# Performance work log

Hardware: AMD Instinct MI355X
Metric: run time of the kernel (lower is better)

The kernel has to match this reference:

```python
import jax, jax.numpy as jnp
import numpy as np
from jax import lax

D_MODEL = 128; HEADS = 4; HEAD_DIM = 32
D_INNER = 256; STATE = 16; KCONV = 4; DT_RANK = 8
N_T = 2; N_M = 6
B = 4; L = 2048; D_IN = 256
EPS = 1e-5


def build_layer_schedule(nt, nm):
    total = nt + nm
    sched = []
    t = 0
    for i in range(total):
        tgt = (i + 1) * nt / total
        if t < tgt and t < nt:
            sched.append('transformer'); t += 1
        else:
            sched.append('mamba')
    return sched


def ln(x, s, b):
    mu = x.mean(-1, keepdims=True)
    v = ((x - mu) ** 2).mean(-1, keepdims=True)
    return (x - mu) * lax.rsqrt(v + EPS) * s + b


def transformer_layer(h, in_w, in_b, out_w, out_b, w1, b1, w2, b2, n1s, n1b, n2s, n2b):
    # torch TransformerEncoderLayer, batch_first, post-norm, relu, dropout=eval(off)
    Bb, S, D = h.shape
    qkv = h @ in_w.T + in_b
    q, k, v = jnp.split(qkv, 3, axis=-1)
    def heads(t):
        return t.reshape(Bb, S, HEADS, HEAD_DIM).transpose(0, 2, 1, 3)
    q, k, v = heads(q), heads(k), heads(v)
    scores = jnp.einsum('bhqd,bhkd->bhqk', q, k) / np.float32(np.sqrt(HEAD_DIM))
    attn = jax.nn.softmax(scores, axis=-1)
    o = jnp.einsum('bhqk,bhkd->bhqd', attn, v).transpose(0, 2, 1, 3).reshape(Bb, S, D)
    o = o @ out_w.T + out_b
    h = ln(h + o, n1s, n1b)
    ff = jax.nn.relu(h @ w1.T + b1) @ w2.T + b2
    return ln(h + ff, n2s, n2b)


def mamba_block(h, ns, nb, in_w, conv_w, conv_b, xp_w, dt_w, dt_b, A_log, Dp, out_w):
    xn = ln(h, ns, nb)
    xz = xn @ in_w.T  # [B,L,2*Di]
    x, z = jnp.split(xz, 2, axis=-1)
    Lseq = x.shape[1]
    # causal depthwise conv1d (pad left K-1, truncate to L)
    xpad = jnp.pad(x, ((0, 0), (KCONV - 1, 0), (0, 0)))
    x = sum(xpad[:, k:k + Lseq, :] * conv_w[:, k] for k in range(KCONV)) + conv_b
    x = jax.nn.silu(x)
    # input-dependent dt, B, C
    dbc = x @ xp_w.T  # [B,L,R+2N]
    dt_r = dbc[..., :DT_RANK]
    Bm = dbc[..., DT_RANK:DT_RANK + STATE]
    Cm = dbc[..., DT_RANK + STATE:]
    dt = jax.nn.softplus(dt_r @ dt_w.T + dt_b)  # [B,L,Di]
    A = -jnp.exp(A_log)  # [Di,N]
    dA = jnp.exp(dt[..., None] * A)               # [B,L,Di,N]
    dBu = (dt * x)[..., None] * Bm[:, :, None, :]  # [B,L,Di,N]

    def step(hstate, inp):
        dA_t, dBu_t, C_t = inp
        hstate = dA_t * hstate + dBu_t
        return hstate, jnp.einsum('bdn,bn->bd', hstate, C_t)

    h0 = jnp.zeros((x.shape[0], D_INNER, STATE), x.dtype)
    _, ys = lax.scan(step, h0, (dA.swapaxes(0, 1), dBu.swapaxes(0, 1), Cm.swapaxes(0, 1)))
    y = ys.swapaxes(0, 1) + x * Dp
    y = y * jax.nn.silu(z)
    return h + y @ out_w.T


def setup_inputs() -> dict:
    key = jax.random.key(0)
    ks = jax.random.split(key, 12)
    def rn(k, shape, s=0.02):
        return jax.random.normal(k, shape, dtype=jnp.float32) * s
    return {
        'x': jax.random.normal(ks[0], (B, L, D_IN), dtype=jnp.float32),
        'proj_w': rn(ks[1], (D_MODEL, D_IN)),
        'proj_b': jnp.zeros((D_MODEL,), jnp.float32),
        't_in_w': rn(ks[2], (N_T, 3 * D_MODEL, D_MODEL)),
        't_in_b': jnp.zeros((N_T, 3 * D_MODEL), jnp.float32),
        't_out_w': rn(ks[3], (N_T, D_MODEL, D_MODEL)),
        't_out_b': jnp.zeros((N_T, D_MODEL), jnp.float32),
        't_ff1_w': rn(ks[4], (N_T, 4 * D_MODEL, D_MODEL)),
        't_ff1_b': jnp.zeros((N_T, 4 * D_MODEL), jnp.float32),
        't_ff2_w': rn(ks[5], (N_T, D_MODEL, 4 * D_MODEL)),
        't_ff2_b': jnp.zeros((N_T, D_MODEL), jnp.float32),
        't_n1_s': jnp.ones((N_T, D_MODEL), jnp.float32),
        't_n1_b': jnp.zeros((N_T, D_MODEL), jnp.float32),
        't_n2_s': jnp.ones((N_T, D_MODEL), jnp.float32),
        't_n2_b': jnp.zeros((N_T, D_MODEL), jnp.float32),
        'm_norm_s': jnp.ones((N_M, D_MODEL), jnp.float32),
        'm_norm_b': jnp.zeros((N_M, D_MODEL), jnp.float32),
        'm_in_w': rn(ks[6], (N_M, 2 * D_INNER, D_MODEL)),
        'm_conv_w': rn(ks[7], (N_M, D_INNER, KCONV), 0.2),
        'm_conv_b': jnp.zeros((N_M, D_INNER), jnp.float32),
        'm_xproj_w': rn(ks[8], (N_M, DT_RANK + 2 * STATE, D_INNER)),
        'm_dt_w': rn(ks[9], (N_M, D_INNER, DT_RANK)),
        'm_dt_b': jnp.full((N_M, D_INNER), -2.0, jnp.float32),
        'm_A_log': jnp.log(jnp.broadcast_to(jnp.arange(1, STATE + 1, dtype=jnp.float32), (N_M, D_INNER, STATE))),
        'm_D': jnp.ones((N_M, D_INNER), jnp.float32),
        'm_out_w': rn(ks[10], (N_M, D_MODEL, D_INNER)),
        'norm_s': jnp.ones((D_MODEL,), jnp.float32),
        'norm_b': jnp.zeros((D_MODEL,), jnp.float32),
    }


def reference(x, proj_w, proj_b, t_in_w, t_in_b, t_out_w, t_out_b, t_ff1_w, t_ff1_b, t_ff2_w, t_ff2_b, t_n1_s, t_n1_b, t_n2_s, t_n2_b, m_norm_s, m_norm_b, m_in_w, m_conv_w, m_conv_b, m_xproj_w, m_dt_w, m_dt_b, m_A_log, m_D, m_out_w, norm_s, norm_b):
    h = x @ proj_w.T + proj_b
    ti = mi = 0
    for kind in build_layer_schedule(N_T, N_M):
        if kind == 'transformer':
            h = transformer_layer(h, t_in_w[ti], t_in_b[ti], t_out_w[ti], t_out_b[ti], t_ff1_w[ti], t_ff1_b[ti], t_ff2_w[ti], t_ff2_b[ti], t_n1_s[ti], t_n1_b[ti], t_n2_s[ti], t_n2_b[ti])
            ti += 1
        else:
            h = mamba_block(h, m_norm_s[mi], m_norm_b[mi], m_in_w[mi], m_conv_w[mi], m_conv_b[mi], m_xproj_w[mi], m_dt_w[mi], m_dt_b[mi], m_A_log[mi], m_D[mi], m_out_w[mi])
            mi += 1
    return ln(h, norm_s, norm_b)
```

## Files before the change

kernel.cpp:

```cpp
#include <hip/hip_runtime.h>
#include <hip/hip_bf16.h>
#include <math.h>

using bf16 = __hip_bfloat16;

typedef __attribute__((ext_vector_type(8))) short short8;
typedef __attribute__((ext_vector_type(4))) short short4v;
typedef __attribute__((ext_vector_type(4))) float float4v;

#define BATCH 4
#define SEQL 2048
#define TOK (BATCH * SEQL)
#define NCHUNK 128
#define TCHUNK 16
#define PSOFF ((size_t)BATCH * NCHUNK * 256 * 16)
#define NSPLIT 2

#define NPAR 28
#define PAR_TOTAL 3227264

struct Srcs { const void* p[NPAR]; int off[NPAR + 1]; };

__device__ __forceinline__ short f2b(float f) {
    unsigned u = __builtin_bit_cast(unsigned, f);
    unsigned r = (u + 0x7FFF + ((u >> 16) & 1)) >> 16;
    return (short)r;
}
__device__ __forceinline__ float b2f(short s) {
    unsigned u = ((unsigned)(unsigned short)s) << 16;
    return __builtin_bit_cast(float, u);
}
__device__ __forceinline__ unsigned pk2t(float a, float b) {
    unsigned ua = __builtin_bit_cast(unsigned, a);
    unsigned ub = __builtin_bit_cast(unsigned, b);
    return (ub & 0xFFFF0000u) | (ua >> 16);
}

__global__ __launch_bounds__(128) void sniff_kernel(const unsigned int* __restrict__ xw,
                                                    int* __restrict__ flag) {
    __shared__ int cnt;
    if (threadIdx.x == 0) cnt = 0;
    __syncthreads();
    unsigned u = xw[threadIdx.x];
    unsigned elo = (u >> 7) & 0xFF;
    unsigned ehi = (u >> 23) & 0xFF;
    int ok = (elo >= 100 && elo <= 140) && (ehi >= 100 && ehi <= 140);
    if (ok) atomicAdd(&cnt, 1);
    __syncthreads();
    if (threadIdx.x == 0) *flag = (cnt >= 96) ? 1 : 0;
}

__global__ __launch_bounds__(256) void cvt_all(Srcs s, const int* __restrict__ flag,
                                               short* __restrict__ dstb, int total) {
    int idx = blockIdx.x * 256 + threadIdx.x;
    if (idx >= total) return;
    int t = 0;
    while (idx >= s.off[t + 1]) ++t;
    int j = idx - s.off[t];
    dstb[idx] = (*flag) ? ((const short*)s.p[t])[j]
                        : f2b(((const float*)s.p[t])[j]);
}

__global__ __launch_bounds__(256) void gemm_gen(const short* __restrict__ A,
                                                const short* __restrict__ W,
                                                const short* __restrict__ bias,
                                                short* __restrict__ Cb,
                                                int N, int K, int lda, int act) {
    __shared__ short As[64][72];
    __shared__ short Bs[64][72];
    const int bm = blockIdx.y * 64, bn = blockIdx.x * 64;
    const int tid = threadIdx.x;
    const int w = tid >> 6, lane = tid & 63;
    const int la = lane & 15, quad = lane >> 4;
    const int srow = tid >> 2, sk0 = (tid & 3) * 16;
    short8 av0, av1, bv0, bv1;
    {
        const short* ap = A + (size_t)(bm + srow) * lda + sk0;
        const short* wp = W + (size_t)(bn + srow) * K + sk0;
        av0 = *(const short8*)ap;
        av1 = *(const short8*)(ap + 8);
        bv0 = *(const short8*)wp;
        bv1 = *(const short8*)(wp + 8);
    }
    float4v acc[4] = {};
    #pragma unroll 1
    for (int kb = 0; kb < K; kb += 64) {
        *(short4v*)&As[srow][sk0]      = *(short4v*)&av0;
        *(short4v*)&As[srow][sk0 + 4]  = *((short4v*)&av0 + 1);
        *(short4v*)&As[srow][sk0 + 8]  = *(short4v*)&av1;
        *(short4v*)&As[srow][sk0 + 12] = *((short4v*)&av1 + 1);
        *(short4v*)&Bs[srow][sk0]      = *(short4v*)&bv0;
        *(short4v*)&Bs[srow][sk0 + 4]  = *((short4v*)&bv0 + 1);
        *(short4v*)&Bs[srow][sk0 + 8]  = *(short4v*)&bv1;
        *(short4v*)&Bs[srow][sk0 + 12] = *((short4v*)&bv1 + 1);
        __syncthreads();
        if (kb + 64 < K) {
            const short* ap = A + (size_t)(bm + srow) * lda + kb + 64 + sk0;
            const short* wp = W + (size_t)(bn + srow) * K + kb + 64 + sk0;
            av0 = *(const short8*)ap;
            av1 = *(const short8*)(ap + 8);
            bv0 = *(const short8*)wp;
            bv1 = *(const short8*)(wp + 8);
        }
        #pragma unroll
        for (int ks = 0; ks < 2; ++ks) {
            short8 af;
            *(short4v*)&af       = *(short4v*)&As[w * 16 + la][ks * 32 + quad * 8];
            *((short4v*)&af + 1) = *(short4v*)&As[w * 16 + la][ks * 32 + quad * 8 + 4];
            #pragma unroll
            for (int f = 0; f < 4; ++f) {
                short8 bf;
                *(short4v*)&bf       = *(short4v*)&Bs[f * 16 + la][ks * 32 + quad * 8];
                *((short4v*)&bf + 1) = *(short4v*)&Bs[f * 16 + la][ks * 32 + quad * 8 + 4];
                acc[f] = __builtin_amdgcn_mfma_f32_16x16x32_bf16(af, bf, acc[f], 0, 0, 0);
            }
        }
        __syncthreads();
    }
    #pragma unroll
    for (int f = 0; f < 4; ++f) {
        int n = bn + f * 16 + la;
        float bv = bias ? b2f(bias[n]) : 0.f;
        #pragma unroll
        for (int i = 0; i < 4; ++i) {
            int m = bm + w * 16 + quad * 4 + i;
            float v = acc[f][i] + bv;
            if (act == 1) v = fmaxf(v, 0.f);
            Cb[(size_t)m * N + n] = f2b(v);
        }
    }
}

__global__ __launch_bounds__(256) void gemm128(const short* __restrict__ A,
                                               const short* __restrict__ W,
                                               const short* __restrict__ bias,
                                               const float* __restrict__ res,
                                               const short* __restrict__ s1,
                                               const short* __restrict__ b1,
                                               const short* __restrict__ s2,
                                               const short* __restrict__ b2,
                                               float* __restrict__ outH,
                                               short* __restrict__ outHb,
                                               short* __restrict__ outX,
                                               int K, int lda,
                                               const short* __restrict__ OpSrc,
                                               const float* __restrict__ ML) {
    __shared__ short As[32][72];
    __shared__ short Bs[128][72];
    __shared__ short Ac[32][136];
    __shared__ float pS[2][34];
    __shared__ float pQ[2][34];
    const int bm = blockIdx.x * 32;
    const int tid = threadIdx.x;
    const int w = tid >> 6, lane = tid & 63;
    const int la = lane & 15, quad = lane >> 4;
    const int wr = w & 1, wc = w >> 1;
    if (OpSrc) {
        const int row = tid >> 3, c0 = (tid & 7) * 16;
        const int tok = bm + row;
        float den = 0.f;
        #pragma unroll
        for (int s = 0; s < NSPLIT; ++s) den += ML[(size_t)s * TOK + tok];
        const float inv = 1.f / den;
        #pragma unroll
        for (int cc = 0; cc < 16; cc += 8) {
            float num[8] = {};
            #pragma unroll
            for (int s = 0; s < NSPLIT; ++s) {
                short8 v = *(const short8*)(OpSrc + ((size_t)s * TOK + tok) * 128 + c0 + cc);
                #pragma unroll
                for (int j = 0; j < 8; ++j) num[j] += b2f(v[j]);
            }
            #pragma unroll
            for (int j = 0; j < 8; ++j) Ac[row][c0 + cc + j] = f2b(num[j] * inv);
        }
        __syncthreads();
    }
    const int br = tid >> 1, bh2 = (tid & 1) * 32;
    short8 breg[4];
    {
        const short* wp = W + (size_t)br * K + bh2;
        #pragma unroll
        for (int j = 0; j < 4; ++j) breg[j] = *(const short8*)(wp + j * 8);
    }
    float4v acc[4] = {};
    #pragma unroll 1
    for (int kb = 0; kb < K; kb += 64) {
        if (!OpSrc) {
            const int row = tid >> 3, k0 = (tid & 7) * 8;
            const short* ap = A + (size_t)(bm + row) * lda + kb + k0;
            short8 a0 = *(const short8*)ap;
            *(short4v*)&As[row][k0]     = *(short4v*)&a0;
            *(short4v*)&As[row][k0 + 4] = *((short4v*)&a0 + 1);
        }
        #pragma unroll
        for (int j = 0; j < 4; ++j) {
            *(short4v*)&Bs[br][bh2 + j * 8]     = *(short4v*)&breg[j];
            *(short4v*)&Bs[br][bh2 + j * 8 + 4] = *((short4v*)&breg[j] + 1);
        }
        __syncthreads();
        if (kb + 64 < K) {
            const short* wp = W + (size_t)br * K + kb + 64 + bh2;
            #pragma unroll
            for (int j = 0; j < 4; ++j) breg[j] = *(const short8*)(wp + j * 8);
        }
        #pragma unroll
        for (int ks = 0; ks < 2; ++ks) {
            short8 af;
            if (OpSrc) {
                *(short4v*)&af       = *(short4v*)&Ac[wr * 16 + la][kb + ks * 32 + quad * 8];
                *((short4v*)&af + 1) = *(short4v*)&Ac[wr * 16 + la][kb + ks * 32 + quad * 8 + 4];
            } else {
                *(short4v*)&af       = *(short4v*)&As[wr * 16 + la][ks * 32 + quad * 8];
                *((short4v*)&af + 1) = *(short4v*)&As[wr * 16 + la][ks * 32 + quad * 8 + 4];
            }
            #pragma unroll
            for (int f = 0; f < 4; ++f) {
                int n = wc * 64 + f * 16 + la;
                short8 bf;
                *(short4v*)&bf       = *(short4v*)&Bs[n][ks * 32 + quad * 8];
                *((short4v*)&bf + 1) = *(short4v*)&Bs[n][ks * 32 + quad * 8 + 4];
                acc[f] = __builtin_amdgcn_mfma_f32_16x16x32_bf16(af, bf, acc[f], 0, 0, 0);
            }
        }
        __syncthreads();
    }
    float v[4][4];
    #pragma unroll
    for (int f = 0; f < 4; ++f) {
        int col = wc * 64 + f * 16 + la;
        float bv = bias ? b2f(bias[col]) : 0.f;
        #pragma unroll
        for (int i = 0; i < 4; ++i) {
            int m = bm + wr * 16 + quad * 4 + i;
            float x = acc[f][i] + bv;
            if (res) x += res[(size_t)m * 128 + col];
            v[f][i] = x;
        }
    }
    float mu_i[4], rs_i[4];
    if (s1 || s2) {
        #pragma unroll
        for (int i = 0; i < 4; ++i) {
            float s = 0.f;
            #pragma unroll
            for (int f = 0; f < 4; ++f) s += v[f][i];
            s += __shfl_xor(s, 1); s += __shfl_xor(s, 2);
            s += __shfl_xor(s, 4); s += __shfl_xor(s, 8);
            if (la == 0) pS[wc][wr * 16 + quad * 4 + i] = s;
        }
        __syncthreads();
        #pragma unroll
        for (int i = 0; i < 4; ++i) {
            int r = wr * 16 + quad * 4 + i;
            mu_i[i] = (pS[0][r] + pS[1][r]) * (1.f / 128.f);
            float q = 0.f;
            #pragma unroll
            for (int f = 0; f < 4; ++f) { float d = v[f][i] - mu_i[i]; q += d * d; }
            q += __shfl_xor(q, 1); q += __shfl_xor(q, 2);
            q += __shfl_xor(q, 4); q += __shfl_xor(q, 8);
            if (la == 0) pQ[wc][r] = q;
        }
        __syncthreads();
        #pragma unroll
        for (int i = 0; i < 4; ++i) {
            int r = wr * 16 + quad * 4 + i;
            rs_i[i] = rsqrtf((pQ[0][r] + pQ[1][r]) * (1.f / 128.f) + 1e-5f);
        }
    }
    #pragma unroll
    for (int f = 0; f < 4; ++f) {
        int col = wc * 64 + f * 16 + la;
        float s1v = s1 ? b2f(s1[col]) : 0.f, b1v = s1 ? b2f(b1[col]) : 0.f;
        float s2v = s2 ? b2f(s2[col]) : 0.f, b2v = s2 ? b2f(b2[col]) : 0.f;
        #pragma unroll
        for (int i = 0; i < 4; ++i) {
            size_t m = bm + wr * 16 + quad * 4 + i;
            float raw = v[f][i];
            float o = s1 ? ((raw - mu_i[i]) * rs_i[i] * s1v + b1v) : raw;
            if (outH)  outH[m * 128 + col] = o;
            if (outHb) outHb[m * 128 + col] = f2b(o);
            if (outX)  outX[m * 128 + col] =
                f2b((raw - mu_i[i]) * rs_i[i] * s2v + b2v);
        }
    }
}

#define FSTR 524
__global__ __launch_bounds__(256) void gemm_ff(const short* __restrict__ A,
                                               const short* __restrict__ W1,
                                               const short* __restrict__ b1,
                                               const short* __restrict__ W2,
                                               const short* __restrict__ b2c,
                                               const float* __restrict__ res,
                                               const short* __restrict__ s1,
                                               const short* __restrict__ b1n,
                                               const short* __restrict__ s2,
                                               const short* __restrict__ b2n,
                                               float* __restrict__ outH,
                                               short* __restrict__ outHb,
                                               short* __restrict__ outX) {
    __shared__ short As[32][136];
    __shared__ short Fs[32][FSTR];
    __shared__ short Bsu[9216];
    __shared__ float pS[2][34];
    __shared__ float pQ[2][34];
    const int bm = blockIdx.x * 32;
    const int tid = threadIdx.x;
    const int w = tid >> 6, lane = tid & 63;
    const int la = lane & 15, quad = lane >> 4;
    const int wr = w & 1, wc = w >> 1;
    {
        const int row = tid >> 3, k0 = (tid & 7) * 16;
        const short* ap = A + (size_t)(bm + row) * 128 + k0;
        #pragma unroll
        for (int j = 0; j < 2; ++j) {
            short8 v = *(const short8*)(ap + j * 8);
            *(short4v*)&As[row][k0 + j * 8]     = *(short4v*)&v;
            *(short4v*)&As[row][k0 + j * 8 + 4] = *((short4v*)&v + 1);
        }
    }
    const int r1 = tid >> 2, h1 = (tid & 3) * 32;
    short8 wreg[4];
    {
        const short* wp = W1 + (size_t)r1 * 128 + h1;
        #pragma unroll
        for (int j = 0; j < 4; ++j) wreg[j] = *(const short8*)(wp + j * 8);
    }
    #pragma unroll 1
    for (int bn = 0; bn < 512; bn += 64) {
        #pragma unroll
        for (int j = 0; j < 4; ++j) {
            *(short4v*)&Bsu[r1 * 136 + h1 + j * 8]     = *(short4v*)&wreg[j];
            *(short4v*)&Bsu[r1 * 136 + h1 + j * 8 + 4] = *((short4v*)&wreg[j] + 1);
        }
        __syncthreads();
        if (bn + 64 < 512) {
            const short* wp = W1 + (size_t)(bn + 64 + r1) * 128 + h1;
            #pragma unroll
            for (int j = 0; j < 4; ++j) wreg[j] = *(const short8*)(wp + j * 8);
        }
        float4v acc1[2] = {};
        #pragma unroll
        for (int ks = 0; ks < 4; ++ks) {
            short8 af;
            *(short4v*)&af       = *(short4v*)&As[wr * 16 + la][ks * 32 + quad * 8];
            *((short4v*)&af + 1) = *(short4v*)&As[wr * 16 + la][ks * 32 + quad * 8 + 4];
            #pragma unroll
            for (int f = 0; f < 2; ++f) {
                short8 bf;
                *(short4v*)&bf       = *(short4v*)&Bsu[((wc * 2 + f) * 16 + la) * 136 + ks * 32 + quad * 8];
                *((short4v*)&bf + 1) = *(short4v*)&Bsu[((wc * 2 + f) * 16 + la) * 136 + ks * 32 + quad * 8 + 4];
                acc1[f] = __builtin_amdgcn_mfma_f32_16x16x32_bf16(af, bf, acc1[f], 0, 0, 0);
            }
        }
        #pragma unroll
        for (int f = 0; f < 2; ++f) {
            int col = bn + (wc * 2 + f) * 16 + la;
            float bv = b2f(b1[col]);
            #pragma unroll
            for (int i = 0; i < 4; ++i) {
                int r = wr * 16 + quad * 4 + i;
                Fs[r][col] = f2b(fmaxf(acc1[f][i] + bv, 0.f));
            }
        }
        __syncthreads();
    }
    const int r2 = tid >> 1, h2 = (tid & 1) * 32;
    {
        const short* wp = W2 + (size_t)r2 * 512 + h2;
        #pragma unroll
        for (int j = 0; j < 4; ++j) wreg[j] = *(const short8*)(wp + j * 8);
    }
    float4v acc[4] = {};
    #pragma unroll 1
    for (int kb = 0; kb < 512; kb += 64) {
        #pragma unroll
        for (int j = 0; j < 4; ++j) {
            *(short4v*)&Bsu[r2 * 72 + h2 + j * 8]     = *(short4v*)&wreg[j];
            *(short4v*)&Bsu[r2 * 72 + h2 + j * 8 + 4] = *((short4v*)&wreg[j] + 1);
        }
        __syncthreads();
        if (kb + 64 < 512) {
            const short* wp = W2 + (size_t)r2 * 512 + kb + 64 + h2;
            #pragma unroll
            for (int j = 0; j < 4; ++j) wreg[j] = *(const short8*)(wp + j * 8);
        }
        #pragma unroll
        for (int ks = 0; ks < 2; ++ks) {
            short8 af;
            *(short4v*)&af       = *(short4v*)&Fs[wr * 16 + la][kb + ks * 32 + quad * 8];
            *((short4v*)&af + 1) = *(short4v*)&Fs[wr * 16 + la][kb + ks * 32 + quad * 8 + 4];
            #pragma unroll
            for (int f = 0; f < 4; ++f) {
                int n = wc * 64 + f * 16 + la;
                short8 bf;
                *(short4v*)&bf       = *(short4v*)&Bsu[n * 72 + ks * 32 + quad * 8];
                *((short4v*)&bf + 1) = *(short4v*)&Bsu[n * 72 + ks * 32 + quad * 8 + 4];
                acc[f] = __builtin_amdgcn_mfma_f32_16x16x32_bf16(af, bf, acc[f], 0, 0, 0);
            }
        }
        __syncthreads();
    }
    float v[4][4];
    #pragma unroll
    for (int f = 0; f < 4; ++f) {
        int col = wc * 64 + f * 16 + la;
        float bv = b2f(b2c[col]);
        #pragma unroll
        for (int i = 0; i < 4; ++i) {
            int m = bm + wr * 16 + quad * 4 + i;
            v[f][i] = acc[f][i] + bv + res[(size_t)m * 128 + col];
        }
    }
    float mu_i[4], rs_i[4];
    #pragma unroll
    for (int i = 0; i < 4; ++i) {
        float s = 0.f;
        #pragma unroll
        for (int f = 0; f < 4; ++f) s += v[f][i];
        s += __shfl_xor(s, 1); s += __shfl_xor(s, 2);
        s += __shfl_xor(s, 4); s += __shfl_xor(s, 8);
        if (la == 0) pS[wc][wr * 16 + quad * 4 + i] = s;
    }
    __syncthreads();
    #pragma unroll
    for (int i = 0; i < 4; ++i) {
        int r = wr * 16 + quad * 4 + i;
        mu_i[i] = (pS[0][r] + pS[1][r]) * (1.f / 128.f);
        float q = 0.f;
        #pragma unroll
        for (int f = 0; f < 4; ++f) { float d = v[f][i] - mu_i[i]; q += d * d; }
        q += __shfl_xor(q, 1); q += __shfl_xor(q, 2);
        q += __shfl_xor(q, 4); q += __shfl_xor(q, 8);
        if (la == 0) pQ[wc][r] = q;
    }
    __syncthreads();
    #pragma unroll
    for (int i = 0; i < 4; ++i) {
        int r = wr * 16 + quad * 4 + i;
        rs_i[i] = rsqrtf((pQ[0][r] + pQ[1][r]) * (1.f / 128.f) + 1e-5f);
    }
    #pragma unroll
    for (int f = 0; f < 4; ++f) {
        int col = wc * 64 + f * 16 + la;
        float s1v = b2f(s1[col]), b1v = b2f(b1n[col]);
        float s2v = s2 ? b2f(s2[col]) : 0.f, b2v = s2 ? b2f(b2n[col]) : 0.f;
        #pragma unroll
        for (int i = 0; i < 4; ++i) {
            size_t m = bm + wr * 16 + quad * 4 + i;
            float raw = v[f][i];
            float o = (raw - mu_i[i]) * rs_i[i] * s1v + b1v;
            outH[m * 128 + col] = o;
            if (outHb) outHb[m * 128 + col] = f2b(o);
            if (outX)  outX[m * 128 + col] =
                f2b((raw - mu_i[i]) * rs_i[i] * s2v + b2v);
        }
    }
}

__global__ __launch_bounds__(256) void attn_part(const short* __restrict__ qkv,
                                                 short* __restrict__ Op,
                                                 float* __restrict__ ML) {
    __shared__ short Ks[64][36];
    __shared__ short Vt[32][78];
    __shared__ short Pb[4][16][70];
    const int bh = blockIdx.y, b = bh >> 2, h = bh & 3;
    const int q0 = blockIdx.x * 64;
    const int sp = blockIdx.z;
    const int tid = threadIdx.x, w = tid >> 6, lane = tid & 63;
    const int la = lane & 15, quad = lane >> 4;
    const size_t tokbase = (size_t)b * SEQL;
    const int hcol = h * 32;
    const float SCL2 = 0.17677669529663687f * 1.4426950408889634f;

    short8 qa;
    {
        const short* qp = qkv + (tokbase + q0 + w * 16 + la) * 384 + hcol + quad * 8;
        short8 qr = *(const short8*)qp;
        #pragma unroll
        for (int j = 0; j < 8; ++j) qa[j] = f2b(b2f(qr[j]) * SCL2);
    }
    float4v o0 = {}, o1 = {};
    float l_r = 0.f;

    const int srow = tid >> 2, sd0 = (tid & 3) * 8;
    const int k0 = sp * (SEQL / NSPLIT), k1 = k0 + SEQL / NSPLIT;
    short8 kreg, vreg;
    {
        const short* kp = qkv + (tokbase + k0 + srow) * 384 + 128 + hcol + sd0;
        kreg = *(const short8*)kp;
        const short* vp = qkv + (tokbase + k0 + srow) * 384 + 256 + hcol + sd0;
        vreg = *(const short8*)vp;
    }
    #pragma unroll 1
    for (int kt = k0; kt < k1; kt += 64) {
        {
            *(short4v*)&Ks[srow][sd0]     = *(short4v*)&kreg;
            *(short4v*)&Ks[srow][sd0 + 4] = *((short4v*)&kreg + 1);
            #pragma unroll
            for (int j = 0; j < 8; ++j) Vt[sd0 + j][srow] = vreg[j];
        }
        __syncthreads();
        if (kt + 64 < k1) {
            const short* kp = qkv + (tokbase + kt + 64 + srow) * 384 + 128 + hcol + sd0;
            kreg = *(const short8*)kp;
            const short* vp = qkv + (tokbase + kt + 64 + srow) * 384 + 256 + hcol + sd0;
            vreg = *(const short8*)vp;
        }
        float4v sc[4];
        #pragma unroll
        for (int f = 0; f < 4; ++f) {
            short8 kf;
            *(short4v*)&kf       = *(short4v*)&Ks[f * 16 + la][quad * 8];
            *((short4v*)&kf + 1) = *(short4v*)&Ks[f * 16 + la][quad * 8 + 4];
            float4v z = {};
            sc[f] = __builtin_amdgcn_mfma_f32_16x16x32_bf16(kf, qa, z, 0, 0, 0);
        }
        float rs = 0.f;
        #pragma unroll
        for (int f = 0; f < 4; ++f)
            #pragma unroll
            for (int i = 0; i < 4; ++i) {
                float pp = exp2f(sc[f][i]);
                sc[f][i] = pp; rs += pp;
            }
        rs += __shfl_xor(rs, 16);
        rs += __shfl_xor(rs, 32);
        l_r += rs;
        #pragma unroll
        for (int f = 0; f < 4; ++f) {
            *(unsigned*)&Pb[w][la][f * 16 + quad * 4]     = pk2t(sc[f][0], sc[f][1]);
            *(unsigned*)&Pb[w][la][f * 16 + quad * 4 + 2] = pk2t(sc[f][2], sc[f][3]);
        }
        #pragma unroll
        for (int c = 0; c < 2; ++c) {
            short8 pa;
            *(short4v*)&pa       = *(short4v*)&Pb[w][la][c * 32 + quad * 8];
            *((short4v*)&pa + 1) = *(short4v*)&Pb[w][la][c * 32 + quad * 8 + 4];
            short8 vb0, vb1;
            *(short4v*)&vb0       = *(short4v*)&Vt[la][c * 32 + quad * 8];
            *((short4v*)&vb0 + 1) = *(short4v*)&Vt[la][c * 32 + quad * 8 + 4];
            *(short4v*)&vb1       = *(short4v*)&Vt[16 + la][c * 32 + quad * 8];
            *((short4v*)&vb1 + 1) = *(short4v*)&Vt[16 + la][c * 32 + quad * 8 + 4];
            o0 = __builtin_amdgcn_mfma_f32_16x16x32_bf16(pa, vb0, o0, 0, 0, 0);
            o1 = __builtin_amdgcn_mfma_f32_16x16x32_bf16(pa, vb1, o1, 0, 0, 0);
        }
        __syncthreads();
    }
    #pragma unroll
    for (int i = 0; i < 4; ++i) {
        float lb = __shfl(l_r, quad * 4 + i);
        size_t tok = tokbase + q0 + w * 16 + quad * 4 + i;
        short* op = Op + ((size_t)sp * TOK + tok) * 128 + hcol;
        op[la]      = f2b(o0[i]);
        op[16 + la] = f2b(o1[i]);
        if (la == 0) ML[(size_t)sp * TOK + tok] = lb;
    }
}

__global__ __launch_bounds__(256) void mamba_af(const short* __restrict__ XN,
                                                const short* __restrict__ Win,
                                                const short* __restrict__ convw,
                                                const short* __restrict__ convb,
                                                const short* __restrict__ xpw,
                                                const short* __restrict__ dtw,
                                                const short* __restrict__ dtb,
                                                const short* __restrict__ A_log,
                                                short* __restrict__ Zb,
                                                short* __restrict__ XC,
                                                float* __restrict__ DBC,
                                                short* __restrict__ DT,
                                                float* __restrict__ PS,
                                                float* __restrict__ DSUM) {
    __shared__ short Xs[32][136];
    __shared__ short Ws[64][136];
    __shared__ short Xxs[20][264];
    __shared__ short convS[TCHUNK][264];
    __shared__ float dbcS[TCHUNK][44];
    const int c = blockIdx.x & (NCHUNK - 1);
    const int b = blockIdx.x >> 7;
    const int tid = threadIdx.x;
    const size_t tb = (size_t)b * SEQL + c * TCHUNK;
    const int w = tid >> 6, lane = tid & 63;
    const int la = lane & 15, quad = lane >> 4;
    const int wr = w & 1, wc = w >> 1;
    {
        const int r = tid >> 3, k0 = (tid & 7) * 16;
        if (r < 19) {
            short8 v0 = {}, v1 = {};
            if (c > 0 || r >= 3) {
                const short* ap = XN + (tb - 3 + r) * 128 + k0;
                v0 = *(const short8*)ap;
                v1 = *(const short8*)(ap + 8);
            }
            *(short4v*)&Xs[r][k0]      = *(short4v*)&v0;
            *(short4v*)&Xs[r][k0 + 4]  = *((short4v*)&v0 + 1);
            *(short4v*)&Xs[r][k0 + 8]  = *(short4v*)&v1;
            *(short4v*)&Xs[r][k0 + 12] = *((short4v*)&v1 + 1);
        }
    }
    const int sr = tid >> 2, skk = (tid & 3) * 32;
    short8 wreg[4];
    {
        const short* wp = Win + (size_t)sr * 128 + skk;
        #pragma unroll
        for (int j = 0; j < 4; ++j) wreg[j] = *(const short8*)(wp + j * 8);
    }
    #pragma unroll 1
    for (int bn = 0; bn < 512; bn += 64) {
        #pragma unroll
        for (int j = 0; j < 4; ++j) {
            *(short4v*)&Ws[sr][skk + j * 8]     = *(short4v*)&wreg[j];
            *(short4v*)&Ws[sr][skk + j * 8 + 4] = *((short4v*)&wreg[j] + 1);
        }
        __syncthreads();
        if (bn + 64 < 512) {
            const short* wp = Win + (size_t)(bn + 64 + sr) * 128 + skk;
            #pragma unroll
            for (int j = 0; j < 4; ++j) wreg[j] = *(const short8*)(wp + j * 8);
        }
        float4v acc[2] = {};
        #pragma unroll
        for (int ks = 0; ks < 4; ++ks) {
            short8 af;
            *(short4v*)&af       = *(short4v*)&Xs[wr * 16 + la][ks * 32 + quad * 8];
            *((short4v*)&af + 1) = *(short4v*)&Xs[wr * 16 + la][ks * 32 + quad * 8 + 4];
            #pragma unroll
            for (int f = 0; f < 2; ++f) {
                short8 bf;
                *(short4v*)&bf       = *(short4v*)&Ws[(wc * 2 + f) * 16 + la][ks * 32 + quad * 8];
                *((short4v*)&bf + 1) = *(short4v*)&Ws[(wc * 2 + f) * 16 + la][ks * 32 + quad * 8 + 4];
                acc[f] = __builtin_amdgcn_mfma_f32_16x16x32_bf16(af, bf, acc[f], 0, 0, 0);
            }
        }
        #pragma unroll
        for (int f = 0; f < 2; ++f) {
            int col = bn + (wc * 2 + f) * 16 + la;
            #pragma unroll
            for (int i = 0; i < 4; ++i) {
                int r = wr * 16 + quad * 4 + i;
                short val = f2b(acc[f][i]);
                if (col < 256) {
                    if (r < 19) Xxs[r][col] = val;
                } else {
                    if (r >= 3 && r < 19)
                        Zb[(tb + r - 3) * 256 + (col - 256)] = val;
                }
            }
        }
        __syncthreads();
    }
    {
        const int d = tid;
        const float w0 = b2f(convw[d * 4]), w1 = b2f(convw[d * 4 + 1]);
        const float w2 = b2f(convw[d * 4 + 2]), w3 = b2f(convw[d * 4 + 3]);
        const float cb = b2f(convb[d]);
        float xm3 = b2f(Xxs[0][d]);
        float xm2 = b2f(Xxs[1][d]);
        float xm1 = b2f(Xxs[2][d]);
        #pragma unroll 2
        for (int t = 0; t < TCHUNK; ++t) {
            float xt = b2f(Xxs[3 + t][d]);
            float a = cb + w0 * xm3 + w1 * xm2 + w2 * xm1 + w3 * xt;
            float sv = a / (1.f + __expf(-a));
            short sb = f2b(sv);
            convS[t][d] = sb;
            XC[(tb + t) * 256 + d] = sb;
            xm3 = xm2; xm2 = xm1; xm1 = xt;
        }
    }
    __syncthreads();
    if (w < 3) {
        const int n = w * 16 + la;
        float4v acc3 = {};
        #pragma unroll
        for (int ks = 0; ks < 8; ++ks) {
            short8 af;
            *(short4v*)&af       = *(short4v*)&convS[la][ks * 32 + quad * 8];
            *((short4v*)&af + 1) = *(short4v*)&convS[la][ks * 32 + quad * 8 + 4];
            short8 bfv = {};
            if (n < 40) {
                const short* wp = xpw + n * 256 + ks * 32 + quad * 8;
                *(short4v*)&bfv       = *(const short4v*)wp;
                *((short4v*)&bfv + 1) = *(const short4v*)(wp + 4);
            }
            acc3 = __builtin_amdgcn_mfma_f32_16x16x32_bf16(af, bfv, acc3, 0, 0, 0);
        }
        if (n < 40) {
            #pragma unroll
            for (int i = 0; i < 4; ++i) {
                int m = quad * 4 + i;
                float x = acc3[i];
                dbcS[m][n] = x;
                DBC[(tb + m) * 40 + n] = x;
            }
        }
    }
    __syncthreads();
    {
        const int d = tid;
        short8 wv = *(const short8*)(dtw + d * 8);
        float wrv[8];
        #pragma unroll
        for (int j = 0; j < 8; ++j) wrv[j] = b2f(wv[j]);
        const float bb = b2f(dtb[d]);
        float Av2[16];
        {
            short8 a0 = *(const short8*)(A_log + d * 16);
            short8 a1 = *(const short8*)(A_log + d * 16 + 8);
            #pragma unroll
            for (int j = 0; j < 8; ++j) {
                Av2[j]     = -__expf(b2f(a0[j])) * 1.4426950408889634f;
                Av2[8 + j] = -__expf(b2f(a1[j])) * 1.4426950408889634f;
            }
        }
        float S[16];
        #pragma unroll
        for (int n = 0; n < 16; ++n) S[n] = 0.f;
        float dts = 0.f;
        #pragma unroll 2
        for (int t = 0; t < TCHUNK; ++t) {
            float a = bb;
            #pragma unroll
            for (int j = 0; j < 8; ++j) a += dbcS[t][j] * wrv[j];
            float dtv = (a > 20.f) ? a : __logf(1.f + __expf(a));
            short ds = f2b(dtv);
            dtv = b2f(ds);
            DT[(tb + t) * 256 + d] = ds;
            dts += dtv;
            float dtx = dtv * b2f(convS[t][d]);
            const float4v* Brow = (const float4v*)&dbcS[t][8];
            #pragma unroll
            for (int g = 0; g < 4; ++g) {
                float4v Bv = Brow[g];
                #pragma unroll
                for (int i = 0; i < 4; ++i) {
                    int n = g * 4 + i;
                    float aa = exp2f(dtv * Av2[n]);
                    S[n] = aa * S[n] + dtx * Bv[i];
                }
            }
        }
        float* Sp = PS + (((size_t)b * NCHUNK + c) * 256 + d) * 16;
        #pragma unroll
        for (int g = 0; g < 4; ++g) {
            float4v sv = {S[g * 4], S[g * 4 + 1], S[g * 4 + 2], S[g * 4 + 3]};
            ((float4v*)Sp)[g] = sv;
        }
        DSUM[((size_t)b * NCHUNK + c) * 256 + d] = dts;
    }
}

__global__ __launch_bounds__(256) void scan_b2(const float* __restrict__ PS,
                                               const float* __restrict__ DSUM,
                                               const short* __restrict__ A_log,
                                               short* __restrict__ H0) {
    __shared__ float Pseg[16][17];
    __shared__ float Sseg[16][17];
    const int bd = blockIdx.x;
    const int b = bd >> 8, d = bd & 255;
    const int seg = threadIdx.x >> 4, n = threadIdx.x & 15;
    const float Avn = -__expf(b2f(A_log[d * 16 + n]));
    const int c0 = seg * 8;
    float sv[8], pv[8];
    float h = 0.f, P = 1.f;
    #pragma unroll
    for (int j = 0; j < 8; ++j) {
        size_t oc = ((size_t)b * NCHUNK + c0 + j) * 256 + d;
        float s = PS[oc * 16 + n];
        float p = __expf(Avn * DSUM[oc]);
        sv[j] = s; pv[j] = p;
        h = p * h + s;
        P *= p;
    }
    Pseg[seg][n] = P; Sseg[seg][n] = h;
    __syncthreads();
    float hin = 0.f;
    for (int s2 = 0; s2 < seg; ++s2)
        hin = Pseg[s2][n] * hin + Sseg[s2][n];
    #pragma unroll
    for (int j = 0; j < 8; ++j) {
        size_t oc = ((size_t)b * NCHUNK + c0 + j) * 256 + d;
        H0[oc * 16 + n] = f2b(hin);
        hin = pv[j] * hin + sv[j];
    }
}

__global__ __launch_bounds__(256) void mamba_b(const short* __restrict__ dt,
                                               const short* __restrict__ xc,
                                               const float* __restrict__ dbc,
                                               const short* __restrict__ A_log,
                                               const short* __restrict__ H0,
                                               const short* __restrict__ Zb,
                                               const short* __restrict__ Dp,
                                               const short* __restrict__ w_out,
                                               float* __restrict__ outH,
                                               short* __restrict__ outHb,
                                               short* __restrict__ outX,
                                               const short* __restrict__ s2,
                                               const short* __restrict__ b2,
                                               void* __restrict__ outd,
                                               const int* __restrict__ flag) {
    __shared__ float BC[TCHUNK][32];
    __shared__ short Ys[TCHUNK][264];
    __shared__ float Vs[TCHUNK][132];
    const int c = blockIdx.x & (NCHUNK - 1);
    const int b = blockIdx.x >> 7;
    const int tid = threadIdx.x;
    const size_t tb = (size_t)b * SEQL + c * TCHUNK;
    {
        const int d = tid;
        for (int i = tid; i < TCHUNK * 32; i += 256) {
            int t = i >> 5, j = i & 31;
            BC[t][j] = dbc[(tb + t) * 40 + 8 + j];
        }
        float Av2[16];
        {
            short8 a0 = *(const short8*)(A_log + d * 16);
            short8 a1 = *(const short8*)(A_log + d * 16 + 8);
            #pragma unroll
            for (int j = 0; j < 8; ++j) {
                Av2[j]     = -__expf(b2f(a0[j])) * 1.4426950408889634f;
                Av2[8 + j] = -__expf(b2f(a1[j])) * 1.4426950408889634f;
            }
        }
        const float Dv = b2f(Dp[d]);
        float h[16];
        {
            const short* hp = H0 + (((size_t)b * NCHUNK + c) * 256 + d) * 16;
            short8 h0a = *(const short8*)hp;
            short8 h0b = *(const short8*)(hp + 8);
            #pragma unroll
            for (int j = 0; j < 8; ++j) {
                h[j]     = b2f(h0a[j]);
                h[8 + j] = b2f(h0b[j]);
            }
        }
        float dtr[TCHUNK], xr[TCHUNK], zr[TCHUNK];
        #pragma unroll
        for (int t = 0; t < TCHUNK; ++t) {
            dtr[t] = b2f(dt[(tb + t) * 256 + d]);
            xr[t]  = b2f(xc[(tb + t) * 256 + d]);
            zr[t]  = b2f(Zb[(tb + t) * 256 + d]);
        }
        __syncthreads();
        #pragma unroll
        for (int t = 0; t < TCHUNK; ++t) {
            float dtx = dtr[t] * xr[t];
            const float4v* row = (const float4v*)&BC[t][0];
            float acc = 0.f;
            #pragma unroll
            for (int g = 0; g < 4; ++g) {
                float4v Bv = row[g];
                float4v Cv = row[4 + g];
                #pragma unroll
                for (int i = 0; i < 4; ++i) {
                    int n = g * 4 + i;
                    float a = exp2f(dtr[t] * Av2[n]);
                    h[n] = a * h[n] + dtx * Bv[i];
                    acc += h[n] * Cv[i];
                }
            }
            float sz = zr[t] / (1.f + __expf(-zr[t]));
            Ys[t][d] = f2b((acc + xr[t] * Dv) * sz);
        }
    }
    __syncthreads();
    const int w = tid >> 6, lane = tid & 63;
    const int la = lane & 15, quad = lane >> 4;
    float4v acc[2] = {};
    #pragma unroll
    for (int ks = 0; ks < 8; ++ks) {
        short8 af;
        *(short4v*)&af       = *(short4v*)&Ys[la][ks * 32 + quad * 8];
        *((short4v*)&af + 1) = *(short4v*)&Ys[la][ks * 32 + quad * 8 + 4];
        #pragma unroll
        for (int f = 0; f < 2; ++f) {
            int n = (w * 2 + f) * 16 + la;
            short8 bf = *(const short8*)(w_out + (size_t)n * 256 + ks * 32 + quad * 8);
            acc[f] = __builtin_amdgcn_mfma_f32_16x16x32_bf16(af, bf, acc[f], 0, 0, 0);
        }
    }
    #pragma unroll
    for (int f = 0; f < 2; ++f) {
        int col = (w * 2 + f) * 16 + la;
        #pragma unroll
        for (int i = 0; i < 4; ++i) {
            int tr = quad * 4 + i;
            Vs[tr][col] = acc[f][i] + outH[(tb + tr) * 128 + col];
        }
    }
    __syncthreads();
    {
        const int tok = tid >> 4, c8 = (tid & 15) * 8;
        float vv[8];
        #pragma unroll
        for (int j = 0; j < 8; ++j) vv[j] = Vs[tok][c8 + j];
        float mu = 0.f, rstd = 0.f;
        if (outX || outd) {
            float s = 0.f;
            #pragma unroll
            for (int j = 0; j < 8; ++j) s += vv[j];
            s += __shfl_xor(s, 1); s += __shfl_xor(s, 2);
            s += __shfl_xor(s, 4); s += __shfl_xor(s, 8);
            mu = s * (1.f / 128.f);
            float q = 0.f;
            #pragma unroll
            for (int j = 0; j < 8; ++j) { float d2 = vv[j] - mu; q += d2 * d2; }
            q += __shfl_xor(q, 1); q += __shfl_xor(q, 2);
            q += __shfl_xor(q, 4); q += __shfl_xor(q, 8);
            rstd = rsqrtf(q * (1.f / 128.f) + 1e-5f);
        }
        size_t m = tb + tok;
        const int fl = outd ? *flag : 0;
        #pragma unroll
        for (int j = 0; j < 8; ++j) {
            int col = c8 + j;
            float raw = vv[j];
            outH[m * 128 + col] = raw;
            if (outHb) outHb[m * 128 + col] = f2b(raw);
            if (outX)  outX[m * 128 + col] =
                f2b((raw - mu) * rstd * b2f(s2[col]) + b2f(b2[col]));
            if (outd) {
                float o = (raw - mu) * rstd * b2f(s2[col]) + b2f(b2[col]);
                if (fl) ((bf16*)outd)[m * 128 + col] = __float2bfloat16(o);
                else    ((float*)outd)[m * 128 + col] = o;
            }
        }
    }
}

static const int kSizes[NPAR] = {
    2097152, 32768, 128, 98304, 768, 32768, 256, 131072, 1024, 131072, 256,
    256, 256, 256, 256, 768, 768, 393216, 6144, 1536, 61440, 12288, 1536,
    24576, 1536, 196608, 128, 128
};

extern "C" void kernel_launch(void* const* d_in, const int* in_sizes, int n_in,
                              void* d_out, int out_size, void* d_ws, size_t ws_size,
                              hipStream_t stream) {
    Srcs srcs;
    int off[NPAR + 1];
    off[0] = 0;
    for (int i = 0; i < NPAR; ++i) {
        srcs.p[i] = d_in[i];
        off[i + 1] = off[i] + kSizes[i];
        srcs.off[i] = off[i];
    }
    srcs.off[NPAR] = off[NPAR];

    int* FLAG = (int*)d_ws;
    float* fp = (float*)((char*)d_ws + 256);
    float* H    = fp; fp += (size_t)TOK * 128;
    float* DBC  = fp; fp += (size_t)TOK * 40;
    float* PS   = fp; fp += (size_t)PSOFF;
    float* DSUM = fp; fp += (size_t)BATCH * NCHUNK * 256;
    float* ML   = fp; fp += (size_t)NSPLIT * TOK;
    short* q = (short*)fp;
    short* PARB = q; q += (size_t)PAR_TOTAL + 64;
    short* Hb   = q; q += (size_t)TOK * 128 + 64;
    short* XNb  = q; q += (size_t)TOK * 128 + 64;
    short* T1B  = q; q += (size_t)TOK * 512 + 64;
    short* OpB  = q; q += (size_t)NSPLIT * TOK * 128 + 64;
    short* XCb  = q; q += (size_t)TOK * 256 + 64;
    short* DTb  = q; q += (size_t)TOK * 256 + 64;
    short* Zb   = q; q += (size_t)TOK * 256 + 64;
    short* H0b  = q; q += (size_t)PSOFF + 64;

    hipLaunchKernelGGL(sniff_kernel, dim3(1), dim3(128), 0, stream,
                       (const unsigned int*)d_in[0], FLAG);
    hipLaunchKernelGGL(cvt_all, dim3((PAR_TOTAL + 255) / 256), dim3(256), 0, stream,
                       srcs, FLAG, PARB, PAR_TOTAL);

    const short* Bx        = PARB + off[0];
    const short* Bproj_w   = PARB + off[1];
    const short* Bproj_b   = PARB + off[2];
    const short* Bt_in_w   = PARB + off[3];
    const short* Bt_in_b   = PARB + off[4];
    const short* Bt_out_w  = PARB + off[5];
    const short* Bt_out_b  = PARB + off[6];
    const short* Bt_ff1_w  = PARB + off[7];
    const short* Bt_ff1_b  = PARB + off[8];
    const short* Bt_ff2_w  = PARB + off[9];
    const short* Bt_ff2_b  = PARB + off[10];
    const short* Bt_n1_s   = PARB + off[11];
    const short* Bt_n1_b   = PARB + off[12];
    const short* Bt_n2_s   = PARB + off[13];
    const short* Bt_n2_b   = PARB + off[14];
    const short* Bm_norm_s = PARB + off[15];
    const short* Bm_norm_b = PARB + off[16];
    const short* Bm_in_w   = PARB + off[17];
    const short* Bm_conv_w = PARB + off[18];
    const short* Bm_conv_b = PARB + off[19];
    const short* Bm_xproj_w= PARB + off[20];
    const short* Bm_dt_w   = PARB + off[21];
    const short* Bm_dt_b   = PARB + off[22];
    const short* Bm_A_log  = PARB + off[23];
    const short* Bm_D      = PARB + off[24];
    const short* Bm_out_w  = PARB + off[25];
    const short* Bnorm_s   = PARB + off[26];
    const short* Bnorm_b   = PARB + off[27];

    hipLaunchKernelGGL(gemm128, dim3(TOK / 32), dim3(256), 0, stream,
                       Bx, Bproj_w, Bproj_b, (const float*)nullptr,
                       (const short*)nullptr, (const short*)nullptr,
                       (const short*)nullptr, (const short*)nullptr,
                       H, Hb, (short*)nullptr, 256, 256,
                       (const short*)nullptr, (const float*)nullptr);

    const char sched[9] = "TMMMTMMM";
    int ti = 0, mi = 0;
    for (int li = 0; li < 8; ++li) {
        char next = (li < 7) ? sched[li + 1] : 'F';
        if (sched[li] == 'T') {
            hipLaunchKernelGGL(gemm_gen, dim3(6, TOK / 64), dim3(256), 0, stream,
                               Hb, Bt_in_w + (size_t)ti * 384 * 128,
                               Bt_in_b + ti * 384, T1B, 384, 128, 128, 0);
            hipLaunchKernelGGL(attn_part, dim3(SEQL / 64, 16, NSPLIT), dim3(256),
                               0, stream, T1B, OpB, ML);
            hipLaunchKernelGGL(gemm128, dim3(TOK / 32), dim3(256), 0, stream,
                               (const short*)nullptr,
                               Bt_out_w + (size_t)ti * 128 * 128,
                               Bt_out_b + ti * 128, H,
                               Bt_n1_s + ti * 128, Bt_n1_b + ti * 128,
                               (const short*)nullptr, (const short*)nullptr,
                               H, Hb, (short*)nullptr, 128, 128, OpB, ML);
            hipLaunchKernelGGL(gemm_ff, dim3(TOK / 32), dim3(256), 0, stream,
                               Hb, Bt_ff1_w + (size_t)ti * 512 * 128,
                               Bt_ff1_b + ti * 512,
                               Bt_ff2_w + (size_t)ti * 128 * 512,
                               Bt_ff2_b + ti * 128, H,
                               Bt_n2_s + ti * 128, Bt_n2_b + ti * 128,
                               (next == 'M') ? Bm_norm_s + mi * 128 : (const short*)nullptr,
                               (next == 'M') ? Bm_norm_b + mi * 128 : (const short*)nullptr,
                               H, Hb, (next == 'M') ? XNb : (short*)nullptr);
            ++ti;
        } else {
            hipLaunchKernelGGL(mamba_af, dim3(BATCH * NCHUNK), dim3(256), 0, stream,
                               XNb, Bm_in_w + (size_t)mi * 512 * 128,
                               Bm_conv_w + mi * 256 * 4, Bm_conv_b + mi * 256,
                               Bm_xproj_w + (size_t)mi * 40 * 256,
                               Bm_dt_w + (size_t)mi * 256 * 8, Bm_dt_b + mi * 256,
                               Bm_A_log + (size_t)mi * 256 * 16,
                               Zb, XCb, DBC, DTb, PS, DSUM);
            hipLaunchKernelGGL(scan_b2, dim3(BATCH * 256), dim3(256), 0, stream,
                               PS, DSUM, Bm_A_log + (size_t)mi * 256 * 16, H0b);
            bool last = (li == 7);
            hipLaunchKernelGGL(mamba_b, dim3(BATCH * NCHUNK), dim3(256), 0, stream,
                               DTb, XCb, DBC, Bm_A_log + (size_t)mi * 256 * 16, H0b,
                               Zb, Bm_D + mi * 256,
                               Bm_out_w + (size_t)mi * 128 * 256,
                               H, (next == 'T') ? Hb : (short*)nullptr,
                               (next == 'M') ? XNb : (short*)nullptr,
                               last ? Bnorm_s : ((next == 'M') ? Bm_norm_s + (mi + 1) * 128 : (const short*)nullptr),
                               last ? Bnorm_b : ((next == 'M') ? Bm_norm_b + (mi + 1) * 128 : (const short*)nullptr),
                               last ? d_out : (void*)nullptr, FLAG);
            ++mi;
        }
    }
}
```

Baseline: 590.0 us.

## Split mamba_b state dimension across two threads and use 512-thread blocks

Each channel's 16-element SSM state is now split across two adjacent threads, with the partial C-dot products combined by a lane shuffle, and the block size doubles to 512. The MFMA out-projection gives each of the 8 waves one 16-column tile, and the LayerNorm epilogue gives each thread 4 columns with an extra shuffle step. The aim is more parallelism and lower per-thread register use in the serial scan, since the grid of 512 blocks is small. In exchange each thread redundantly loads dt, x and z, and the shuffle and branch add overhead.

New measurement: 582.6 us (median of 2 runs). Within noise of the previous version (-1.3%).

```diff
diff --git a/kernel.cpp b/kernel.cpp
--- a/kernel.cpp
+++ b/kernel.cpp
@@ -787,7 +787,7 @@
     }
 }
 
-__global__ __launch_bounds__(256) void mamba_b(const short* __restrict__ dt,
+__global__ __launch_bounds__(512) void mamba_b(const short* __restrict__ dt,
                                                const short* __restrict__ xc,
                                                const float* __restrict__ dbc,
                                                const short* __restrict__ A_log,
@@ -810,32 +810,25 @@
     const int tid = threadIdx.x;
     const size_t tb = (size_t)b * SEQL + c * TCHUNK;
     {
-        const int d = tid;
-        for (int i = tid; i < TCHUNK * 32; i += 256) {
-            int t = i >> 5, j = i & 31;
+        const int d = tid >> 1, hf = tid & 1;
+        {
+            int t = tid >> 5, j = tid & 31;
             BC[t][j] = dbc[(tb + t) * 40 + 8 + j];
         }
-        float Av2[16];
+        float Av2[8];
         {
-            short8 a0 = *(const short8*)(A_log + d * 16);
-            short8 a1 = *(const short8*)(A_log + d * 16 + 8);
-            #pragma unroll
-            for (int j = 0; j < 8; ++j) {
-                Av2[j]     = -__expf(b2f(a0[j])) * 1.4426950408889634f;
-                Av2[8 + j] = -__expf(b2f(a1[j])) * 1.4426950408889634f;
-            }
+            short8 a0 = *(const short8*)(A_log + d * 16 + hf * 8);
+            #pragma unroll
+            for (int j = 0; j < 8; ++j)
+                Av2[j] = -__expf(b2f(a0[j])) * 1.4426950408889634f;
         }
         const float Dv = b2f(Dp[d]);
-        float h[16];
+        float h[8];
         {
-            const short* hp = H0 + (((size_t)b * NCHUNK + c) * 256 + d) * 16;
+            const short* hp = H0 + (((size_t)b * NCHUNK + c) * 256 + d) * 16 + hf * 8;
             short8 h0a = *(const short8*)hp;
-            short8 h0b = *(const short8*)(hp + 8);
-            #pragma unroll
-            for (int j = 0; j < 8; ++j) {
-                h[j]     = b2f(h0a[j]);
-                h[8 + j] = b2f(h0b[j]);
-            }
+            #pragma unroll
+            for (int j = 0; j < 8; ++j) h[j] = b2f(h0a[j]);
         }
         float dtr[TCHUNK], xr[TCHUNK], zr[TCHUNK];
         #pragma unroll
@@ -848,12 +841,13 @@
         #pragma unroll
         for (int t = 0; t < TCHUNK; ++t) {
             float dtx = dtr[t] * xr[t];
-            const float4v* row = (const float4v*)&BC[t][0];
+            const float4v* rowB = (const float4v*)&BC[t][hf * 8];
+            const float4v* rowC = (const float4v*)&BC[t][16 + hf * 8];
             float acc = 0.f;
             #pragma unroll
-            for (int g = 0; g < 4; ++g) {
-                float4v Bv = row[g];
-                float4v Cv = row[4 + g];
+            for (int g = 0; g < 2; ++g) {
+                float4v Bv = rowB[g];
+                float4v Cv = rowC[g];
                 #pragma unroll
                 for (int i = 0; i < 4; ++i) {
                     int n = g * 4 + i;
@@ -862,61 +856,62 @@
                     acc += h[n] * Cv[i];
                 }
             }
-            float sz = zr[t] / (1.f + __expf(-zr[t]));
-            Ys[t][d] = f2b((acc + xr[t] * Dv) * sz);
+            acc += __shfl_xor(acc, 1);
+            if (hf == 0) {
+                float sz = zr[t] / (1.f + __expf(-zr[t]));
+                Ys[t][d] = f2b((acc + xr[t] * Dv) * sz);
+            }
         }
     }
     __syncthreads();
     const int w = tid >> 6, lane = tid & 63;
     const int la = lane & 15, quad = lane >> 4;
-    float4v acc[2] = {};
+    float4v acc2 = {};
     #pragma unroll
     for (int ks = 0; ks < 8; ++ks) {
         short8 af;
         *(short4v*)&af       = *(short4v*)&Ys[la][ks * 32 + quad * 8];
         *((short4v*)&af + 1) = *(short4v*)&Ys[la][ks * 32 + quad * 8 + 4];
-        #pragma unroll
-        for (int f = 0; f < 2; ++f) {
-            int n = (w * 2 + f) * 16 + la;
-            short8 bf = *(const short8*)(w_out + (size_t)n * 256 + ks * 32 + quad * 8);
-            acc[f] = __builtin_amdgcn_mfma_f32_16x16x32_bf16(af, bf, acc[f], 0, 0, 0);
-        }
-    }
-    #pragma unroll
-    for (int f = 0; f < 2; ++f) {
-        int col = (w * 2 + f) * 16 + la;
+        int n = w * 16 + la;
+        short8 bf = *(const short8*)(w_out + (size_t)n * 256 + ks * 32 + quad * 8);
+        acc2 = __builtin_amdgcn_mfma_f32_16x16x32_bf16(af, bf, acc2, 0, 0, 0);
+    }
+    {
+        int col = w * 16 + la;
         #pragma unroll
         for (int i = 0; i < 4; ++i) {
             int tr = quad * 4 + i;
-            Vs[tr][col] = acc[f][i] + outH[(tb + tr) * 128 + col];
+            Vs[tr][col] = acc2[i] + outH[(tb + tr) * 128 + col];
         }
     }
     __syncthreads();
     {
-        const int tok = tid >> 4, c8 = (tid & 15) * 8;
-        float vv[8];
-        #pragma unroll
-        for (int j = 0; j < 8; ++j) vv[j] = Vs[tok][c8 + j];
+        const int tok = tid >> 5, c4 = (tid & 31) * 4;
+        float vv[4];
+        #pragma unroll
+        for (int j = 0; j < 4; ++j) vv[j] = Vs[tok][c4 + j];
         float mu = 0.f, rstd = 0.f;
         if (outX || outd) {
             float s = 0.f;
             #pragma unroll
-            for (int j = 0; j < 8; ++j) s += vv[j];
+            for (int j = 0; j < 4; ++j) s += vv[j];
             s += __shfl_xor(s, 1); s += __shfl_xor(s, 2);
             s += __shfl_xor(s, 4); s += __shfl_xor(s, 8);
+            s += __shfl_xor(s, 16);
             mu = s * (1.f / 128.f);
             float q = 0.f;
             #pragma unroll
-            for (int j = 0; j < 8; ++j) { float d2 = vv[j] - mu; q += d2 * d2; }
+            for (int j = 0; j < 4; ++j) { float d2 = vv[j] - mu; q += d2 * d2; }
             q += __shfl_xor(q, 1); q += __shfl_xor(q, 2);
             q += __shfl_xor(q, 4); q += __shfl_xor(q, 8);
+            q += __shfl_xor(q, 16);
             rstd = rsqrtf(q * (1.f / 128.f) + 1e-5f);
         }
         size_t m = tb + tok;
         const int fl = outd ? *flag : 0;
         #pragma unroll
-        for (int j = 0; j < 8; ++j) {
-            int col = c8 + j;
+        for (int j = 0; j < 4; ++j) {
+            int col = c4 + j;
             float raw = vv[j];
             outH[m * 128 + col] = raw;
             if (outHb) outHb[m * 128 + col] = f2b(raw);
@@ -1047,7 +1042,7 @@
             hipLaunchKernelGGL(scan_b2, dim3(BATCH * 256), dim3(256), 0, stream,
                                PS, DSUM, Bm_A_log + (size_t)mi * 256 * 16, H0b);
             bool last = (li == 7);
-            hipLaunchKernelGGL(mamba_b, dim3(BATCH * NCHUNK), dim3(256), 0, stream,
+            hipLaunchKernelGGL(mamba_b, dim3(BATCH * NCHUNK), dim3(512), 0, stream,
                                DTb, XCb, DBC, Bm_A_log + (size_t)mi * 256 * 16, H0b,
                                Zb, Bm_D + mi * 256,
                                Bm_out_w + (size_t)mi * 128 * 256,
```
